# Kernel tuning notes

Hardware: AMD Instinct MI355X
Metric: run time of the kernel (lower is better)

Reference implementation:

```python
import jax, jax.numpy as jnp
import numpy as np

G, N, EPG = 32, 128, 2048   # graphs, nodes/graph (uniform), edges/graph
H, L = 128, 2               # hidden_dim, num_layers
OUT = 12


def setup_inputs() -> dict:
    key = jax.random.key(0)
    ks = jax.random.split(key, 32)
    x = jax.random.randint(ks[0], (G * N, 9), 0, 2, dtype=jnp.int32)
    edge_attr = jax.random.randint(ks[1], (G * EPG, 3), 0, 2, dtype=jnp.int32)
    # edges stay within their own graph (global ids = local + graph offset)
    src = jax.random.randint(ks[2], (G, EPG), 0, N, dtype=jnp.int32)
    dst = jax.random.randint(ks[3], (G, EPG), 0, N, dtype=jnp.int32)
    off = (jnp.arange(G, dtype=jnp.int32) * N)[:, None]
    edge_index = jnp.stack([(src + off).reshape(-1), (dst + off).reshape(-1)]).astype(jnp.int64)
    batch_idx = (jnp.arange(G * N) // N).astype(jnp.int32)

    def p(k, shape, scale=0.05):
        return jax.random.normal(k, shape, dtype=jnp.float32) * scale

    return dict(
        x=x, edge_index=edge_index, edge_attr=edge_attr, batch_idx=batch_idx,
        atom_tab=p(ks[4], (9, 119, H)), bond_tab=p(ks[5], (3, 8, H)),
        W_m1=p(ks[6], (L, 2 * H, H)), b_m1=jnp.zeros((L, H), jnp.float32),
        W_m2=p(ks[7], (L, 2 * H, H)), b_m2=jnp.zeros((L, H), jnp.float32),
        W_me=p(ks[8], (L, H, H)), b_me=jnp.zeros((L, H), jnp.float32),
        W_mg=p(ks[9], (L, H, H)), b_mg=jnp.zeros((L, H), jnp.float32),
        W_h1=p(ks[10], (L, H, H)), b_h1=jnp.zeros((L, H), jnp.float32),
        W_h2=p(ks[11], (L, H, H)), b_h2=jnp.zeros((L, H), jnp.float32),
        W_o1=p(ks[12], (L, 2 * H, H)), b_o1=jnp.zeros((L, H), jnp.float32),
        W_o2=p(ks[13], (L, H, H)), b_o2=jnp.zeros((L, H), jnp.float32),
        Wg1=p(ks[14], (H, H)), bg1=jnp.zeros((H,), jnp.float32),
        Wg2=p(ks[15], (H, OUT)), bg2=jnp.zeros((OUT,), jnp.float32),
    )


def reference(x, edge_index, edge_attr, batch_idx, atom_tab, bond_tab,
              W_m1, b_m1, W_m2, b_m2, W_me, b_me, W_mg, b_mg,
              W_h1, b_h1, W_h2, b_h2, W_o1, b_o1, W_o2, b_o2,
              Wg1, bg1, Wg2, bg2):
    # Atom/Bond encoders: sum of per-feature embeddings
    node_fts = jnp.sum(jax.vmap(lambda t, i: t[i], in_axes=(0, 1))(atom_tab, x), axis=0)        # (G*N, H)
    edge_fts = jnp.sum(jax.vmap(lambda t, i: t[i], in_axes=(0, 1))(bond_tab, edge_attr), axis=0)  # (E, H)

    # dense adjacency + dense edge features (one fused scatter, replaces per-graph loop)
    g = (edge_index[0] // N).astype(jnp.int32)
    s = (edge_index[0] % N).astype(jnp.int32)
    d = (edge_index[1] % N).astype(jnp.int32)
    adj = jnp.zeros((G, N, N), jnp.float32).at[g, s, d].set(1.0)
    edense = jnp.zeros((G, N, N, H), jnp.float32).at[g, s, d].set(edge_fts)

    nd = node_fts.reshape(G, N, H)          # to_dense_batch (uniform graphs -> no padding)
    gf = jnp.zeros((G, H), jnp.float32)
    hid = jnp.zeros_like(nd)
    NEG = jnp.float32(-1e9)

    for l in range(L):  # CLRS MPNN layers
        z = jnp.concatenate([nd, hid], axis=-1)                 # (G, N, 2H)
        m1 = z @ W_m1[l] + b_m1[l]
        m2 = z @ W_m2[l] + b_m2[l]
        me = edense @ W_me[l] + b_me[l]                         # (G, N, N, H)
        mg = gf @ W_mg[l] + b_mg[l]
        msgs = m1[:, None, :, :] + m2[:, :, None, :] + me + mg[:, None, None, :]
        h = jax.nn.relu(msgs)
        h = jax.nn.relu(h @ W_h1[l] + b_h1[l]) @ W_h2[l] + b_h2[l]
        h = jnp.where(adj[..., None] > 0, h, NEG)               # masked max over senders
        agg = jnp.max(h, axis=1)                                # (G, N, H)
        hid = jax.nn.relu(z @ W_o1[l] + b_o1[l] + agg @ W_o2[l] + b_o2[l])

    emb = hid.mean(axis=1)                                      # (G, H)
    return jax.nn.relu(emb @ Wg1 + bg1) @ Wg2 + bg2             # (G, OUT)
```

## Files before the change

### kernel.cpp

```cpp
#include <hip/hip_runtime.h>

#define Gg   32
#define Nn   128
#define Hh   128
#define Ee   65536
#define GN   4096
#define GNN  524288

typedef unsigned short ushort_t;
typedef __attribute__((ext_vector_type(8))) __bf16 bf16x8;
typedef __attribute__((ext_vector_type(4))) float f32x4;
struct us4 { ushort_t a, b, c, d; };

__device__ __forceinline__ float reluf(float x) { return x > 0.f ? x : 0.f; }

__device__ __forceinline__ unsigned fkey(float f) {
  unsigned u = __float_as_uint(f);
  return (u & 0x80000000u) ? ~u : (u | 0x80000000u);
}
__device__ __forceinline__ float funkey(unsigned k) {
  unsigned u = (k & 0x80000000u) ? (k ^ 0x80000000u) : ~k;
  return __uint_as_float(u);
}

__device__ __forceinline__ ushort_t bfh(float x) {
  unsigned u = __float_as_uint(x);
  return (ushort_t)((u + 0x7FFFu + ((u >> 16) & 1u)) >> 16);
}
__device__ __forceinline__ void split2(float x, ushort_t& h, ushort_t& l) {
  h = bfh(x);
  float hf = __uint_as_float(((unsigned)h) << 16);
  l = bfh(x - hf);
}

__global__ __launch_bounds__(128) void k_detect(const int* __restrict__ e32,
                                                int* __restrict__ flag) {
  __shared__ int s;
  if (threadIdx.x == 0) s = 0;
  __syncthreads();
  if (e32[2 * threadIdx.x + 1] != 0) atomicOr(&s, 1);
  __syncthreads();
  if (threadIdx.x == 0) *flag = s;
}

__global__ __launch_bounds__(256) void k_bond_fts(const float* __restrict__ bond_tab,
                                                  float* __restrict__ bf) {
  int t = blockIdx.x * 256 + threadIdx.x;
  int c = t >> 7, h = t & 127;
  int a0 = c & 7, a1 = (c >> 3) & 7, a2 = (c >> 6) & 7;
  bf[t] = bond_tab[(0 * 8 + a0) * Hh + h] + bond_tab[(1 * 8 + a1) * Hh + h] +
          bond_tab[(2 * 8 + a2) * Hh + h];
}

__global__ __launch_bounds__(256) void k_scatter_win(const int* __restrict__ e32,
                                                     const int* __restrict__ flag,
                                                     int* __restrict__ win) {
  int e = blockIdx.x * 256 + threadIdx.x;
  int sg, dg;
  if (*flag) { sg = e32[e]; dg = e32[Ee + e]; }
  else       { sg = e32[2 * e]; dg = e32[2 * Ee + 2 * e]; }
  int g = sg / Nn;
  int s = sg % Nn;
  int d = dg % Nn;
  atomicMax(&win[(g * Nn + d) * Nn + s], e);
}

__global__ __launch_bounds__(256) void k_dcount(const int* __restrict__ win,
                                                int* __restrict__ dcnt) {
  int tid = threadIdx.x;
  int grp = tid >> 7, t = tid & 127;
  int dest = blockIdx.x * 2 + grp;
  bool valid = win[dest * 128 + t] >= 0;
  unsigned long long mask = __ballot(valid);
  __shared__ int cw[4];
  if ((tid & 63) == 0) cw[tid >> 6] = __popcll(mask);
  __syncthreads();
  if (t == 0) dcnt[dest] = cw[grp * 2] + cw[grp * 2 + 1];
}

__global__ __launch_bounds__(512) void k_dscan(const int* __restrict__ dcnt,
                                               int* __restrict__ rowptr) {
  int tid = threadIdx.x;
  int c0, c1, c2, c3, c4, c5, c6, c7;
  int bi = tid * 8;
  c0 = dcnt[bi + 0]; c1 = dcnt[bi + 1]; c2 = dcnt[bi + 2]; c3 = dcnt[bi + 3];
  c4 = dcnt[bi + 4]; c5 = dcnt[bi + 5]; c6 = dcnt[bi + 6]; c7 = dcnt[bi + 7];
  int s = c0 + c1 + c2 + c3 + c4 + c5 + c6 + c7;
  int x = s;
#pragma unroll
  for (int off = 1; off < 64; off <<= 1) {
    int y = __shfl_up(x, off, 64);
    if ((tid & 63) >= off) x += y;
  }
  __shared__ int wsum[8], woff[8];
  if ((tid & 63) == 63) wsum[tid >> 6] = x;
  __syncthreads();
  if (tid == 0) {
    int a = 0;
#pragma unroll
    for (int i = 0; i < 8; ++i) { woff[i] = a; a += wsum[i]; }
  }
  __syncthreads();
  int base = x - s + woff[tid >> 6];
  rowptr[bi + 0] = base; base += c0;
  rowptr[bi + 1] = base; base += c1;
  rowptr[bi + 2] = base; base += c2;
  rowptr[bi + 3] = base; base += c3;
  rowptr[bi + 4] = base; base += c4;
  rowptr[bi + 5] = base; base += c5;
  rowptr[bi + 6] = base; base += c6;
  rowptr[bi + 7] = base; base += c7;
  if (tid == 511) rowptr[4096] = base;
}

__global__ __launch_bounds__(256) void k_dfill(const int* __restrict__ win,
                                               const int* __restrict__ eattr,
                                               const int* __restrict__ rowptr,
                                               unsigned* __restrict__ recs) {
  int tid = threadIdx.x;
  int grp = tid >> 7, t = tid & 127;
  int dest = blockIdx.x * 2 + grp;
  int e = win[dest * 128 + t];
  bool valid = e >= 0;
  unsigned long long mask = __ballot(valid);
  __shared__ int cw[4];
  int lane = tid & 63;
  if (lane == 0) cw[tid >> 6] = __popcll(mask);
  __syncthreads();
  if (valid) {
    int off = __popcll(mask & ((1ull << lane) - 1));
    if ((tid >> 6) & 1) off += cw[grp * 2];
    int a0 = eattr[e * 3 + 0], a1 = eattr[e * 3 + 1], a2 = eattr[e * 3 + 2];
    unsigned code = (unsigned)(a0 + (a1 << 3) + (a2 << 6));
    unsigned idx = ((unsigned)dest << 7) | (unsigned)t;
    recs[rowptr[dest] + off] = (idx << 9) | code;
  }
}


__global__ __launch_bounds__(256) void k_wprep(const float* __restrict__ W_h1,
                                               const float* __restrict__ W_h2,
                                               ushort_t* __restrict__ wt) {
  int t = blockIdx.x * 256 + threadIdx.x;
  int l = t >> 15;
  int m = (t >> 14) & 1;
  int e = t & 16383;
  int n = e & 127, k = e >> 7;
  const float* W = (m == 0 ? W_h1 : W_h2) + l * 16384;
  float v = W[k * 128 + n];
  ushort_t h, lo;
  split2(v, h, lo);
  int nf = n >> 4, lr = n & 15, kf = k >> 5, lg = (k >> 3) & 3, j = k & 7;
  int off = ((nf * 4 + kf) * 64 + lg * 16 + lr) * 8 + j;
  int base = ((l * 2 + m) * 2) * 16384;
  wt[base + off] = h;
  wt[base + 16384 + off] = lo;
}

__global__ __launch_bounds__(256) void k_wprep_o(const float* __restrict__ W_o1,
                                                 const float* __restrict__ W_o2,
                                                 ushort_t* __restrict__ wo) {
  int e = blockIdx.x * 256 + threadIdx.x;
  int l = blockIdx.y;
  int n = e / 384, k = e - n * 384;
  float v = (k < 256) ? W_o1[(l * 256 + k) * 128 + n]
                      : W_o2[(l * 128 + (k - 256)) * 128 + n];
  ushort_t h, lo;
  split2(v, h, lo);
  int nf = n >> 4, lr = n & 15, kf = k >> 5, lg = (k >> 3) & 3, j = k & 7;
  int off = ((nf * 12 + kf) * 64 + lg * 16 + lr) * 8 + j;
  wo[(l * 2 + 0) * 49152 + off] = h;
  wo[(l * 2 + 1) * 49152 + off] = lo;
}

__global__ __launch_bounds__(256) void k_wprep_m(const float* __restrict__ W_m1,
                                                 const float* __restrict__ W_m2,
                                                 ushort_t* __restrict__ wm) {
  int t = blockIdx.x * 256 + threadIdx.x;
  int l = t >> 16;
  int m = (t >> 15) & 1;
  int e = t & 32767;
  int n = e >> 8, k = e & 255;
  const float* W = (m == 0 ? W_m1 : W_m2);
  float v = W[(l * 256 + k) * 128 + n];
  ushort_t h, lo;
  split2(v, h, lo);
  int nf = n >> 4, lr = n & 15, kf = k >> 5, lg = (k >> 3) & 3, j = k & 7;
  int off = ((nf * 8 + kf) * 64 + lg * 16 + lr) * 8 + j;
  int base = ((l * 2 + m) * 2) * 32768;
  wm[base + off] = h;
  wm[base + 32768 + off] = lo;
}

__global__ __launch_bounds__(256) void k_me2(const float* __restrict__ bf,
                                             const float* __restrict__ W_me,
                                             const float* __restrict__ b_me,
                                             const float* __restrict__ b_mg,
                                             float* __restrict__ me0,
                                             float* __restrict__ me1,
                                             unsigned* __restrict__ aggkA,
                                             unsigned* __restrict__ aggkB) {
  int bx = blockIdx.x;
  int l = bx >> 8, b2 = bx & 255;
  const float* W = W_me + l * 16384;
  const float* bme = b_me + l * 128;
  const float* bmg = b_mg + l * 128;
  float* me = l ? me1 : me0;
  unsigned* aggk = l ? aggkB : aggkA;
  __shared__ float v[2][128];
  int tid = threadIdx.x;
  int half = tid >> 7, j = tid & 127;
  int c = b2 * 2 + half;
  v[half][j] = bf[c * 128 + j];
  __syncthreads();
  float acc = bme[j] + bmg[j];
  for (int i = 0; i < 128; ++i) acc += v[half][i] * W[i * 128 + j];
  me[c * 128 + j] = acc;
  unsigned key = fkey(-1.0e9f);
#pragma unroll
  for (int i = 0; i < 8; ++i) aggk[b2 * 2048 + i * 256 + tid] = key;
}

__device__ __forceinline__ void load_afrag(const ushort_t (*MH)[136],
                                           const ushort_t (*ML)[136],
                                           int row, int lg,
                                           bf16x8 ah[4], bf16x8 al[4]) {
#pragma unroll
  for (int kf = 0; kf < 4; ++kf) {
    ah[kf] = *(const bf16x8*)&MH[row][lg * 8 + 32 * kf];
    al[kf] = *(const bf16x8*)&ML[row][lg * 8 + 32 * kf];
  }
}

__device__ __forceinline__ void load_afrag264(const ushort_t (*MH)[264],
                                              const ushort_t (*ML)[264],
                                              int row, int base, int lg,
                                              bf16x8 ah[4], bf16x8 al[4]) {
#pragma unroll
  for (int kf = 0; kf < 4; ++kf) {
    ah[kf] = *(const bf16x8*)&MH[row][base + lg * 8 + 32 * kf];
    al[kf] = *(const bf16x8*)&ML[row][base + lg * 8 + 32 * kf];
  }
}

__global__ __launch_bounds__(256) void k_encode_m12(const int* __restrict__ x,
                                                    const float* __restrict__ atom_tab,
                                                    const ushort_t* __restrict__ wm,
                                                    const float* __restrict__ bi1,
                                                    const float* __restrict__ bi2,
                                                    float* __restrict__ nf_,
                                                    float* __restrict__ hid,
                                                    float* __restrict__ m1,
                                                    float* __restrict__ m2) {
  __shared__ ushort_t AH[16][136];
  __shared__ ushort_t AL[16][136];
  __shared__ int xs[144];
  int tid = threadIdx.x;
  int v0 = blockIdx.x * 16;
  if (tid < 144) xs[tid] = x[v0 * 9 + tid];
  __syncthreads();
#pragma unroll
  for (int i = 0; i < 8; ++i) {
    int e = tid + i * 256;
    int row = e >> 7, col = e & 127;
    float s = 0.f;
#pragma unroll
    for (int f = 0; f < 9; ++f) {
      int idx = xs[row * 9 + f];
      s += atom_tab[(f * 119 + idx) * Hh + col];
    }
    nf_[(v0 + row) * Hh + col] = s;
    hid[(v0 + row) * Hh + col] = 0.f;
    ushort_t h, l;
    split2(s, h, l);
    AH[row][col] = h;
    AL[row][col] = l;
  }
  __syncthreads();
  int lane = tid & 63, wid = tid >> 6;
  int lr = lane & 15, lg = lane >> 4;
  f32x4 a1[2], a2[2];
#pragma unroll
  for (int i = 0; i < 2; ++i) { a1[i] = (f32x4){0.f,0.f,0.f,0.f}; a2[i] = (f32x4){0.f,0.f,0.f,0.f}; }
  const ushort_t* w1h = wm;
  const ushort_t* w1l = wm + 32768;
  const ushort_t* w2h = wm + 65536;
  const ushort_t* w2l = wm + 98304;
  bf16x8 ah[4], al[4];
  load_afrag(AH, AL, lr, lg, ah, al);
#pragma unroll
  for (int jj = 0; jj < 2; ++jj) {
    int nfr = 2 * wid + jj;
#pragma unroll
    for (int kf = 0; kf < 4; ++kf) {
      int ch = ((nfr * 8 + kf) << 9) + lane * 8;
      bf16x8 b1h = *(const bf16x8*)(w1h + ch);
      bf16x8 b1l = *(const bf16x8*)(w1l + ch);
      bf16x8 b2h = *(const bf16x8*)(w2h + ch);
      bf16x8 b2l = *(const bf16x8*)(w2l + ch);
      a1[jj] = __builtin_amdgcn_mfma_f32_16x16x32_bf16(ah[kf], b1h, a1[jj], 0, 0, 0);
      a1[jj] = __builtin_amdgcn_mfma_f32_16x16x32_bf16(ah[kf], b1l, a1[jj], 0, 0, 0);
      a1[jj] = __builtin_amdgcn_mfma_f32_16x16x32_bf16(al[kf], b1h, a1[jj], 0, 0, 0);
      a2[jj] = __builtin_amdgcn_mfma_f32_16x16x32_bf16(ah[kf], b2h, a2[jj], 0, 0, 0);
      a2[jj] = __builtin_amdgcn_mfma_f32_16x16x32_bf16(ah[kf], b2l, a2[jj], 0, 0, 0);
      a2[jj] = __builtin_amdgcn_mfma_f32_16x16x32_bf16(al[kf], b2h, a2[jj], 0, 0, 0);
    }
  }
#pragma unroll
  for (int jj = 0; jj < 2; ++jj) {
    int col = 16 * (2 * wid + jj) + lr;
    float bb1 = bi1[col], bb2 = bi2[col];
#pragma unroll
    for (int reg = 0; reg < 4; ++reg) {
      int row = v0 + lg * 4 + reg;
      m1[row * Hh + col] = a1[jj][reg] + bb1;
      m2[row * Hh + col] = a2[jj][reg] + bb2;
    }
  }
}

__global__ __launch_bounds__(512) void k_edge(const unsigned* __restrict__ recs,
                                              const int* __restrict__ cnt,
                                              const float* __restrict__ m1,
                                              const float* __restrict__ m2,
                                              const float* __restrict__ me,
                                              const ushort_t* __restrict__ wt1h,
                                              const ushort_t* __restrict__ wt1l,
                                              const ushort_t* __restrict__ wt2h,
                                              const ushort_t* __restrict__ wt2l,
                                              const float* __restrict__ b_h1,
                                              const float* __restrict__ b_h2,
                                              unsigned* __restrict__ aggk) {
  __shared__ ushort_t MH[64][136];
  __shared__ ushort_t ML[64][136];
  __shared__ unsigned srec[64];
  int tid = threadIdx.x;
  int n = *cnt;
  if (tid < 64) {
    int r = blockIdx.x * 64 + tid;
    srec[tid] = (r < n) ? recs[r] : 0xFFFFFFFFu;
  }
  __syncthreads();
  {
    int c4 = tid & 31, rq = tid >> 5;
#pragma unroll
    for (int i = 0; i < 4; ++i) {
      int r = 16 * i + rq;
      float4 v = make_float4(0.f, 0.f, 0.f, 0.f);
      unsigned rec = srec[r];
      if (rec != 0xFFFFFFFFu) {
        int code = rec & 511;
        unsigned idx = rec >> 9;
        int s = idx & 127, d = (idx >> 7) & 127, g = idx >> 14;
        float4 a = *(const float4*)(m1 + (((g << 7) + d) << 7) + c4 * 4);
        float4 b = *(const float4*)(m2 + (((g << 7) + s) << 7) + c4 * 4);
        float4 cme = *(const float4*)(me + (code << 7) + c4 * 4);
        v.x = reluf(a.x + b.x + cme.x);
        v.y = reluf(a.y + b.y + cme.y);
        v.z = reluf(a.z + b.z + cme.z);
        v.w = reluf(a.w + b.w + cme.w);
      }
      us4 h4, l4;
      split2(v.x, h4.a, l4.a); split2(v.y, h4.b, l4.b);
      split2(v.z, h4.c, l4.c); split2(v.w, h4.d, l4.d);
      *(us4*)&MH[r][c4 * 4] = h4;
      *(us4*)&ML[r][c4 * 4] = l4;
    }
  }
  __syncthreads();

  int lane = tid & 63, wid = tid >> 6;
  int lr = lane & 15, lg = lane >> 4;
  float b1v = b_h1[16 * wid + lr];
  float b2v = b_h2[16 * wid + lr];
  f32x4 acc[4];
#pragma unroll
  for (int rg = 0; rg < 4; ++rg) acc[rg] = (f32x4){0.f, 0.f, 0.f, 0.f};
#pragma unroll
  for (int rg = 0; rg < 4; ++rg) {
    bf16x8 ah[4], al[4];
    load_afrag(MH, ML, 16 * rg + lr, lg, ah, al);
#pragma unroll
    for (int kf = 0; kf < 4; ++kf) {
      int ch = ((wid * 4 + kf) << 9) + lane * 8;
      bf16x8 bh = *(const bf16x8*)(wt1h + ch);
      bf16x8 bl = *(const bf16x8*)(wt1l + ch);
      acc[rg] = __builtin_amdgcn_mfma_f32_16x16x32_bf16(ah[kf], bh, acc[rg], 0, 0, 0);
      acc[rg] = __builtin_amdgcn_mfma_f32_16x16x32_bf16(ah[kf], bl, acc[rg], 0, 0, 0);
      acc[rg] = __builtin_amdgcn_mfma_f32_16x16x32_bf16(al[kf], bh, acc[rg], 0, 0, 0);
    }
  }
  __syncthreads();
#pragma unroll
  for (int rg = 0; rg < 4; ++rg)
#pragma unroll
    for (int reg = 0; reg < 4; ++reg) {
      float t = reluf(acc[rg][reg] + b1v);
      int row = 16 * rg + lg * 4 + reg;
      int col = 16 * wid + lr;
      ushort_t h, l;
      split2(t, h, l);
      MH[row][col] = h;
      ML[row][col] = l;
    }
  __syncthreads();
#pragma unroll
  for (int rg = 0; rg < 4; ++rg) acc[rg] = (f32x4){0.f, 0.f, 0.f, 0.f};
#pragma unroll
  for (int rg = 0; rg < 4; ++rg) {
    bf16x8 ah[4], al[4];
    load_afrag(MH, ML, 16 * rg + lr, lg, ah, al);
#pragma unroll
    for (int kf = 0; kf < 4; ++kf) {
      int ch = ((wid * 4 + kf) << 9) + lane * 8;
      bf16x8 bh = *(const bf16x8*)(wt2h + ch);
      bf16x8 bl = *(const bf16x8*)(wt2l + ch);
      acc[rg] = __builtin_amdgcn_mfma_f32_16x16x32_bf16(ah[kf], bh, acc[rg], 0, 0, 0);
      acc[rg] = __builtin_amdgcn_mfma_f32_16x16x32_bf16(ah[kf], bl, acc[rg], 0, 0, 0);
      acc[rg] = __builtin_amdgcn_mfma_f32_16x16x32_bf16(al[kf], bh, acc[rg], 0, 0, 0);
    }
  }
  __syncthreads();
#pragma unroll
  for (int rg = 0; rg < 4; ++rg)
#pragma unroll
    for (int reg = 0; reg < 4; ++reg) {
      int row = 16 * rg + lg * 4 + reg;
      int col = 16 * wid + lr;
      unsigned b = __float_as_uint(acc[rg][reg] + b2v);
      MH[row][col] = (ushort_t)(b >> 16);
      ML[row][col] = (ushort_t)(b & 0xFFFFu);
    }
  __syncthreads();
  {
    int c = tid & 127, quarter = tid >> 7;
    int rbeg = quarter * 16, rend = rbeg + 16;
    unsigned curkey = 0xFFFFu;
    float best = -3.0e38f;
    for (int r = rbeg; r < rend; ++r) {
      unsigned rec = srec[r];
      unsigned key = rec >> 16;
      if (key != curkey) {
        if (curkey != 0xFFFFu)
          atomicMax(aggk + (curkey << 7) + c, fkey(best));
        curkey = key;
        best = -3.0e38f;
      }
      if (key != 0xFFFFu) {
        unsigned b = ((unsigned)MH[r][c] << 16) | (unsigned)ML[r][c];
        best = fmaxf(best, __uint_as_float(b));
      }
    }
    if (curkey != 0xFFFFu)
      atomicMax(aggk + (curkey << 7) + c, fkey(best));
  }
}

__global__ __launch_bounds__(256) void k_out(const float* __restrict__ nf,
                                             const float* __restrict__ hid,
                                             const unsigned* __restrict__ aggk,
                                             const ushort_t* __restrict__ wo_h,
                                             const ushort_t* __restrict__ wo_l,
                                             const float* __restrict__ bo1,
                                             const float* __restrict__ bo2,
                                             float* __restrict__ hidn) {
  __shared__ ushort_t MH[16][136];
  __shared__ ushort_t ML[16][136];
  int tid = threadIdx.x;
  int v0 = blockIdx.x * 16;
  int lane = tid & 63, wid = tid >> 6;
  int lr = lane & 15, lg = lane >> 4;
  f32x4 acc[2];
#pragma unroll
  for (int jj = 0; jj < 2; ++jj) acc[jj] = (f32x4){0.f, 0.f, 0.f, 0.f};

  for (int seg = 0; seg < 3; ++seg) {
#pragma unroll
    for (int i = 0; i < 2; ++i) {
      int idx = tid + i * 256;
      int row = idx >> 5, c4 = idx & 31;
      float4 v;
      if (seg == 0)      v = ((const float4*)nf)[(v0 + row) * 32 + c4];
      else if (seg == 1) v = ((const float4*)hid)[(v0 + row) * 32 + c4];
      else {
        uint4 k4 = ((const uint4*)aggk)[(v0 + row) * 32 + c4];
        v.x = funkey(k4.x); v.y = funkey(k4.y); v.z = funkey(k4.z); v.w = funkey(k4.w);
      }
      us4 h4, l4;
      split2(v.x, h4.a, l4.a);
      split2(v.y, h4.b, l4.b);
      split2(v.z, h4.c, l4.c);
      split2(v.w, h4.d, l4.d);
      *(us4*)&MH[row][c4 * 4] = h4;
      *(us4*)&ML[row][c4 * 4] = l4;
    }
    __syncthreads();
    bf16x8 ah[4], al[4];
    load_afrag(MH, ML, lr, lg, ah, al);
#pragma unroll
    for (int jj = 0; jj < 2; ++jj) {
      int nfr = 2 * wid + jj;
#pragma unroll
      for (int kf = 0; kf < 4; ++kf) {
        int ch = ((nfr * 12 + seg * 4 + kf) << 9) + lane * 8;
        bf16x8 bh = *(const bf16x8*)(wo_h + ch);
        bf16x8 bl = *(const bf16x8*)(wo_l + ch);
        acc[jj] = __builtin_amdgcn_mfma_f32_16x16x32_bf16(ah[kf], bh, acc[jj], 0, 0, 0);
        acc[jj] = __builtin_amdgcn_mfma_f32_16x16x32_bf16(ah[kf], bl, acc[jj], 0, 0, 0);
        acc[jj] = __builtin_amdgcn_mfma_f32_16x16x32_bf16(al[kf], bh, acc[jj], 0, 0, 0);
      }
    }
    __syncthreads();
  }
#pragma unroll
  for (int jj = 0; jj < 2; ++jj) {
    int col = 16 * (2 * wid + jj) + lr;
    float b = bo1[col] + bo2[col];
#pragma unroll
    for (int reg = 0; reg < 4; ++reg)
      hidn[(v0 + lg * 4 + reg) * Hh + col] = reluf(acc[jj][reg] + b);
  }
}

__global__ __launch_bounds__(256) void k_out_m12(const float* __restrict__ nf,
                                                 const float* __restrict__ hid,
                                                 const unsigned* __restrict__ aggk,
                                                 const ushort_t* __restrict__ wo_h,
                                                 const ushort_t* __restrict__ wo_l,
                                                 const float* __restrict__ bo1,
                                                 const float* __restrict__ bo2,
                                                 const ushort_t* __restrict__ wm,
                                                 const float* __restrict__ bm1,
                                                 const float* __restrict__ bm2,
                                                 float* __restrict__ hidn,
                                                 float* __restrict__ m1,
                                                 float* __restrict__ m2) {
  __shared__ ushort_t AH[16][264];
  __shared__ ushort_t AL[16][264];
  int tid = threadIdx.x;
  int v0 = blockIdx.x * 16;
  int lane = tid & 63, wid = tid >> 6;
  int lr = lane & 15, lg = lane >> 4;
  f32x4 acc[2];
#pragma unroll
  for (int jj = 0; jj < 2; ++jj) acc[jj] = (f32x4){0.f, 0.f, 0.f, 0.f};

  for (int seg = 0; seg < 3; ++seg) {
#pragma unroll
    for (int i = 0; i < 2; ++i) {
      int idx = tid + i * 256;
      int row = idx >> 5, c4 = idx & 31;
      float4 v;
      if (seg == 0)      v = ((const float4*)nf)[(v0 + row) * 32 + c4];
      else if (seg == 1) v = ((const float4*)hid)[(v0 + row) * 32 + c4];
      else {
        uint4 k4 = ((const uint4*)aggk)[(v0 + row) * 32 + c4];
        v.x = funkey(k4.x); v.y = funkey(k4.y); v.z = funkey(k4.z); v.w = funkey(k4.w);
      }
      us4 h4, l4;
      split2(v.x, h4.a, l4.a);
      split2(v.y, h4.b, l4.b);
      split2(v.z, h4.c, l4.c);
      split2(v.w, h4.d, l4.d);
      *(us4*)&AH[row][c4 * 4] = h4;
      *(us4*)&AL[row][c4 * 4] = l4;
    }
    __syncthreads();
    bf16x8 ah[4], al[4];
    load_afrag264(AH, AL, lr, 0, lg, ah, al);
#pragma unroll
    for (int jj = 0; jj < 2; ++jj) {
      int nfr = 2 * wid + jj;
#pragma unroll
      for (int kf = 0; kf < 4; ++kf) {
        int ch = ((nfr * 12 + seg * 4 + kf) << 9) + lane * 8;
        bf16x8 bh = *(const bf16x8*)(wo_h + ch);
        bf16x8 bl = *(const bf16x8*)(wo_l + ch);
        acc[jj] = __builtin_amdgcn_mfma_f32_16x16x32_bf16(ah[kf], bh, acc[jj], 0, 0, 0);
        acc[jj] = __builtin_amdgcn_mfma_f32_16x16x32_bf16(ah[kf], bl, acc[jj], 0, 0, 0);
        acc[jj] = __builtin_amdgcn_mfma_f32_16x16x32_bf16(al[kf], bh, acc[jj], 0, 0, 0);
      }
    }
    __syncthreads();
  }
#pragma unroll
  for (int jj = 0; jj < 2; ++jj) {
    int col = 16 * (2 * wid + jj) + lr;
    float b = bo1[col] + bo2[col];
#pragma unroll
    for (int reg = 0; reg < 4; ++reg) {
      float hv = reluf(acc[jj][reg] + b);
      int row = lg * 4 + reg;
      hidn[(v0 + row) * Hh + col] = hv;
      ushort_t h, l;
      split2(hv, h, l);
      AH[row][128 + col] = h;
      AL[row][128 + col] = l;
    }
  }
#pragma unroll
  for (int i = 0; i < 2; ++i) {
    int idx = tid + i * 256;
    int row = idx >> 5, c4 = idx & 31;
    float4 v = ((const float4*)nf)[(v0 + row) * 32 + c4];
    us4 h4, l4;
    split2(v.x, h4.a, l4.a);
    split2(v.y, h4.b, l4.b);
    split2(v.z, h4.c, l4.c);
    split2(v.w, h4.d, l4.d);
    *(us4*)&AH[row][c4 * 4] = h4;
    *(us4*)&AL[row][c4 * 4] = l4;
  }
  __syncthreads();
  f32x4 a1[2], a2[2];
#pragma unroll
  for (int i = 0; i < 2; ++i) { a1[i] = (f32x4){0.f,0.f,0.f,0.f}; a2[i] = (f32x4){0.f,0.f,0.f,0.f}; }
  const ushort_t* w1h = wm;
  const ushort_t* w1l = wm + 32768;
  const ushort_t* w2h = wm + 65536;
  const ushort_t* w2l = wm + 98304;
#pragma unroll
  for (int seg = 0; seg < 2; ++seg) {
    bf16x8 ah[4], al[4];
    load_afrag264(AH, AL, lr, seg * 128, lg, ah, al);
#pragma unroll
    for (int jj = 0; jj < 2; ++jj) {
      int nfr = 2 * wid + jj;
#pragma unroll
      for (int kf = 0; kf < 4; ++kf) {
        int ch = ((nfr * 8 + seg * 4 + kf) << 9) + lane * 8;
        bf16x8 b1h = *(const bf16x8*)(w1h + ch);
        bf16x8 b1l = *(const bf16x8*)(w1l + ch);
        bf16x8 b2h = *(const bf16x8*)(w2h + ch);
        bf16x8 b2l = *(const bf16x8*)(w2l + ch);
        a1[jj] = __builtin_amdgcn_mfma_f32_16x16x32_bf16(ah[kf], b1h, a1[jj], 0, 0, 0);
        a1[jj] = __builtin_amdgcn_mfma_f32_16x16x32_bf16(ah[kf], b1l, a1[jj], 0, 0, 0);
        a1[jj] = __builtin_amdgcn_mfma_f32_16x16x32_bf16(al[kf], b1h, a1[jj], 0, 0, 0);
        a2[jj] = __builtin_amdgcn_mfma_f32_16x16x32_bf16(ah[kf], b2h, a2[jj], 0, 0, 0);
        a2[jj] = __builtin_amdgcn_mfma_f32_16x16x32_bf16(ah[kf], b2l, a2[jj], 0, 0, 0);
        a2[jj] = __builtin_amdgcn_mfma_f32_16x16x32_bf16(al[kf], b2h, a2[jj], 0, 0, 0);
      }
    }
  }
#pragma unroll
  for (int jj = 0; jj < 2; ++jj) {
    int col = 16 * (2 * wid + jj) + lr;
    float bb1 = bm1[col], bb2 = bm2[col];
#pragma unroll
    for (int reg = 0; reg < 4; ++reg) {
      int row = v0 + lg * 4 + reg;
      m1[row * Hh + col] = a1[jj][reg] + bb1;
      m2[row * Hh + col] = a2[jj][reg] + bb2;
    }
  }
}

__global__ __launch_bounds__(128) void k_head(const float* __restrict__ hid,
                                              const float* __restrict__ Wg1,
                                              const float* __restrict__ bg1,
                                              const float* __restrict__ Wg2,
                                              const float* __restrict__ bg2,
                                              float* __restrict__ out) {
  __shared__ float emb[Hh];
  __shared__ float tt[Hh];
  int g = blockIdx.x, j = threadIdx.x;
  float s = 0.f;
  for (int n = 0; n < Nn; ++n) s += hid[(g * Nn + n) * Hh + j];
  emb[j] = s * (1.f / Nn);
  __syncthreads();
  float a = bg1[j];
  for (int i = 0; i < Hh; ++i) a += emb[i] * Wg1[i * Hh + j];
  tt[j] = reluf(a);
  __syncthreads();
  if (j < 12) {
    float o = bg2[j];
    for (int i = 0; i < Hh; ++i) o += tt[i] * Wg2[i * 12 + j];
    out[g * 12 + j] = o;
  }
}

extern "C" void kernel_launch(void* const* d_in, const int* in_sizes, int n_in,
                              void* d_out, int out_size, void* d_ws, size_t ws_size,
                              hipStream_t stream) {
  const int* x = (const int*)d_in[0];
  const int* eidx32 = (const int*)d_in[1];
  const int* eattr = (const int*)d_in[2];
  const float* atom_tab = (const float*)d_in[4];
  const float* bond_tab = (const float*)d_in[5];
  const float* W_m1 = (const float*)d_in[6];
  const float* b_m1 = (const float*)d_in[7];
  const float* W_m2 = (const float*)d_in[8];
  const float* b_m2 = (const float*)d_in[9];
  const float* W_me = (const float*)d_in[10];
  const float* b_me = (const float*)d_in[11];
  const float* b_mg = (const float*)d_in[13];
  const float* W_h1 = (const float*)d_in[14];
  const float* b_h1 = (const float*)d_in[15];
  const float* W_h2 = (const float*)d_in[16];
  const float* b_h2 = (const float*)d_in[17];
  const float* W_o1 = (const float*)d_in[18];
  const float* b_o1 = (const float*)d_in[19];
  const float* W_o2 = (const float*)d_in[20];
  const float* b_o2 = (const float*)d_in[21];
  const float* Wg1 = (const float*)d_in[22];
  const float* bg1 = (const float*)d_in[23];
  const float* Wg2 = (const float*)d_in[24];
  const float* bg2 = (const float*)d_in[25];
  float* out = (float*)d_out;

  char* ws = (char*)d_ws;
  float* nf = (float*)(ws);
  float* hidA = (float*)(ws + (2u << 20));
  float* hidB = (float*)(ws + (4u << 20));
  float* m1 = (float*)(ws + (6u << 20));
  float* m2 = (float*)(ws + (8u << 20));
  unsigned* aggkA = (unsigned*)(ws + (10u << 20));
  int* win = (int*)(ws + (12u << 20));
  ushort_t* wt = (ushort_t*)(ws + (14u << 20));
  float* bf = (float*)(ws + (14u << 20) + (256u << 10));
  float* me0 = (float*)(ws + (14u << 20) + (512u << 10));
  float* me1 = (float*)(ws + (14u << 20) + (768u << 10));
  unsigned* recs = (unsigned*)(ws + (15u << 20));
  int* dcnt = (int*)(ws + (15u << 20) + (256u << 10));
  int* rowptr = (int*)(ws + (15u << 20) + (272u << 10));
  int* eflag = (int*)(ws + (15u << 20) + (304u << 10));
  unsigned* aggkB = (unsigned*)(ws + (16u << 20));
  ushort_t* wo = (ushort_t*)(ws + (18u << 20));
  ushort_t* wm = (ushort_t*)(ws + (18u << 20) + (512u << 10));

  hipMemsetAsync(win, 0xFF, GNN * sizeof(int), stream);
  k_detect<<<1, 128, 0, stream>>>(eidx32, eflag);
  k_bond_fts<<<256, 256, 0, stream>>>(bond_tab, bf);
  k_wprep<<<256, 256, 0, stream>>>(W_h1, W_h2, wt);
  k_wprep_o<<<dim3(192, 2), 256, 0, stream>>>(W_o1, W_o2, wo);
  k_wprep_m<<<512, 256, 0, stream>>>(W_m1, W_m2, wm);
  k_me2<<<512, 256, 0, stream>>>(bf, W_me, b_me, b_mg, me0, me1, aggkA, aggkB);
  k_encode_m12<<<256, 256, 0, stream>>>(x, atom_tab, wm, b_m1, b_m2,
                                        nf, hidA, m1, m2);
  k_scatter_win<<<256, 256, 0, stream>>>(eidx32, eflag, win);
  k_dcount<<<2048, 256, 0, stream>>>(win, dcnt);
  k_dscan<<<1, 512, 0, stream>>>(dcnt, rowptr);
  k_dfill<<<2048, 256, 0, stream>>>(win, eattr, rowptr, recs);

  int* cnt = rowptr + 4096;

  k_edge<<<1024, 512, 0, stream>>>(recs, cnt, m1, m2, me0,
                                   wt + 0 * 16384, wt + 1 * 16384,
                                   wt + 2 * 16384, wt + 3 * 16384,
                                   b_h1, b_h2, aggkA);
  k_out_m12<<<256, 256, 0, stream>>>(nf, hidA, aggkA,
                                     wo + 0 * 49152, wo + 1 * 49152,
                                     b_o1, b_o2,
                                     wm + 131072, b_m1 + Hh, b_m2 + Hh,
                                     hidB, m1, m2);
  k_edge<<<1024, 512, 0, stream>>>(recs, cnt, m1, m2, me1,
                                   wt + 4 * 16384, wt + 5 * 16384,
                                   wt + 6 * 16384, wt + 7 * 16384,
                                   b_h1 + Hh, b_h2 + Hh, aggkB);
  k_out<<<256, 256, 0, stream>>>(nf, hidB, aggkB,
                                 wo + 2 * 49152, wo + 3 * 49152,
                                 b_o1 + Hh, b_o2 + Hh, hidA);
  k_head<<<32, 128, 0, stream>>>(hidA, Wg1, bg1, Wg2, bg2, out);
}
```

Measured before the change: 127.6 us.

## Fuse preprocessing kernels and replace count/scan/fill with atomic-append compaction

Merges the three weight-prep kernels and the adjacency-window memset into one launch, and folds the edge-format detection into the scatter kernel and the bond-feature sum into k_me2. It replaces the dcount/dscan/dfill pipeline with a single fill kernel that reserves output slots through an atomicAdd on a global counter. Together these remove several launches and their serialization gaps. In exchange, the record order becomes nondeterministic across runs, and k_edge must tolerate records that are no longer grouped in destination order.

```diff
diff --git a/kernel.cpp b/kernel.cpp
--- a/kernel.cpp
+++ b/kernel.cpp
@@ -33,31 +33,80 @@
   l = bfh(x - hf);
 }
 
-__global__ __launch_bounds__(128) void k_detect(const int* __restrict__ e32,
-                                                int* __restrict__ flag) {
-  __shared__ int s;
-  if (threadIdx.x == 0) s = 0;
-  __syncthreads();
-  if (e32[2 * threadIdx.x + 1] != 0) atomicOr(&s, 1);
-  __syncthreads();
-  if (threadIdx.x == 0) *flag = s;
-}
-
-__global__ __launch_bounds__(256) void k_bond_fts(const float* __restrict__ bond_tab,
-                                                  float* __restrict__ bf) {
-  int t = blockIdx.x * 256 + threadIdx.x;
-  int c = t >> 7, h = t & 127;
-  int a0 = c & 7, a1 = (c >> 3) & 7, a2 = (c >> 6) & 7;
-  bf[t] = bond_tab[(0 * 8 + a0) * Hh + h] + bond_tab[(1 * 8 + a1) * Hh + h] +
-          bond_tab[(2 * 8 + a2) * Hh + h];
+__global__ __launch_bounds__(256) void k_wprep_all(const float* __restrict__ W_h1,
+                                                   const float* __restrict__ W_h2,
+                                                   const float* __restrict__ W_o1,
+                                                   const float* __restrict__ W_o2,
+                                                   const float* __restrict__ W_m1,
+                                                   const float* __restrict__ W_m2,
+                                                   ushort_t* __restrict__ wt,
+                                                   ushort_t* __restrict__ wo,
+                                                   ushort_t* __restrict__ wm,
+                                                   int* __restrict__ win,
+                                                   int* __restrict__ cnt) {
+  int b = blockIdx.x;
+  int tid = threadIdx.x;
+  if (b < 256) {
+    int t = b * 256 + tid;
+    int l = t >> 15;
+    int m = (t >> 14) & 1;
+    int e = t & 16383;
+    int n = e & 127, k = e >> 7;
+    const float* W = (m == 0 ? W_h1 : W_h2) + l * 16384;
+    float v = W[k * 128 + n];
+    ushort_t h, lo;
+    split2(v, h, lo);
+    int nf = n >> 4, lr = n & 15, kf = k >> 5, lg = (k >> 3) & 3, j = k & 7;
+    int off = ((nf * 4 + kf) * 64 + lg * 16 + lr) * 8 + j;
+    int base = ((l * 2 + m) * 2) * 16384;
+    wt[base + off] = h;
+    wt[base + 16384 + off] = lo;
+  } else if (b < 640) {
+    int ep = (b - 256) * 256 + tid;
+    int l = (ep >= 49152) ? 1 : 0;
+    int e = ep - l * 49152;
+    int n = e / 384, k = e - n * 384;
+    float v = (k < 256) ? W_o1[(l * 256 + k) * 128 + n]
+                        : W_o2[(l * 128 + (k - 256)) * 128 + n];
+    ushort_t h, lo;
+    split2(v, h, lo);
+    int nf = n >> 4, lr = n & 15, kf = k >> 5, lg = (k >> 3) & 3, j = k & 7;
+    int off = ((nf * 12 + kf) * 64 + lg * 16 + lr) * 8 + j;
+    wo[(l * 2 + 0) * 49152 + off] = h;
+    wo[(l * 2 + 1) * 49152 + off] = lo;
+  } else if (b < 1152) {
+    int t = (b - 640) * 256 + tid;
+    int l = t >> 16;
+    int m = (t >> 15) & 1;
+    int e = t & 32767;
+    int n = e >> 8, k = e & 255;
+    const float* W = (m == 0 ? W_m1 : W_m2);
+    float v = W[(l * 256 + k) * 128 + n];
+    ushort_t h, lo;
+    split2(v, h, lo);
+    int nf = n >> 4, lr = n & 15, kf = k >> 5, lg = (k >> 3) & 3, j = k & 7;
+    int off = ((nf * 8 + kf) * 64 + lg * 16 + lr) * 8 + j;
+    int base = ((l * 2 + m) * 2) * 32768;
+    wm[base + off] = h;
+    wm[base + 32768 + off] = lo;
+  } else {
+    int idx = (b - 1152) * 256 + tid;
+    ((int4*)win)[idx] = make_int4(-1, -1, -1, -1);
+    if (idx == 0) *cnt = 0;
+  }
 }
 
 __global__ __launch_bounds__(256) void k_scatter_win(const int* __restrict__ e32,
-                                                     const int* __restrict__ flag,
                                                      int* __restrict__ win) {
-  int e = blockIdx.x * 256 + threadIdx.x;
+  __shared__ int sflag;
+  int tid = threadIdx.x;
+  if (tid == 0) sflag = 0;
+  __syncthreads();
+  if (tid < 128 && e32[2 * tid + 1] != 0) atomicOr(&sflag, 1);
+  __syncthreads();
+  int e = blockIdx.x * 256 + tid;
   int sg, dg;
-  if (*flag) { sg = e32[e]; dg = e32[Ee + e]; }
+  if (sflag) { sg = e32[e]; dg = e32[Ee + e]; }
   else       { sg = e32[2 * e]; dg = e32[2 * Ee + 2 * e]; }
   int g = sg / Nn;
   int s = sg % Nn;
@@ -65,58 +114,10 @@
   atomicMax(&win[(g * Nn + d) * Nn + s], e);
 }
 
-__global__ __launch_bounds__(256) void k_dcount(const int* __restrict__ win,
-                                                int* __restrict__ dcnt) {
-  int tid = threadIdx.x;
-  int grp = tid >> 7, t = tid & 127;
-  int dest = blockIdx.x * 2 + grp;
-  bool valid = win[dest * 128 + t] >= 0;
-  unsigned long long mask = __ballot(valid);
-  __shared__ int cw[4];
-  if ((tid & 63) == 0) cw[tid >> 6] = __popcll(mask);
-  __syncthreads();
-  if (t == 0) dcnt[dest] = cw[grp * 2] + cw[grp * 2 + 1];
-}
-
-__global__ __launch_bounds__(512) void k_dscan(const int* __restrict__ dcnt,
-                                               int* __restrict__ rowptr) {
-  int tid = threadIdx.x;
-  int c0, c1, c2, c3, c4, c5, c6, c7;
-  int bi = tid * 8;
-  c0 = dcnt[bi + 0]; c1 = dcnt[bi + 1]; c2 = dcnt[bi + 2]; c3 = dcnt[bi + 3];
-  c4 = dcnt[bi + 4]; c5 = dcnt[bi + 5]; c6 = dcnt[bi + 6]; c7 = dcnt[bi + 7];
-  int s = c0 + c1 + c2 + c3 + c4 + c5 + c6 + c7;
-  int x = s;
-#pragma unroll
-  for (int off = 1; off < 64; off <<= 1) {
-    int y = __shfl_up(x, off, 64);
-    if ((tid & 63) >= off) x += y;
-  }
-  __shared__ int wsum[8], woff[8];
-  if ((tid & 63) == 63) wsum[tid >> 6] = x;
-  __syncthreads();
-  if (tid == 0) {
-    int a = 0;
-#pragma unroll
-    for (int i = 0; i < 8; ++i) { woff[i] = a; a += wsum[i]; }
-  }
-  __syncthreads();
-  int base = x - s + woff[tid >> 6];
-  rowptr[bi + 0] = base; base += c0;
-  rowptr[bi + 1] = base; base += c1;
-  rowptr[bi + 2] = base; base += c2;
-  rowptr[bi + 3] = base; base += c3;
-  rowptr[bi + 4] = base; base += c4;
-  rowptr[bi + 5] = base; base += c5;
-  rowptr[bi + 6] = base; base += c6;
-  rowptr[bi + 7] = base; base += c7;
-  if (tid == 511) rowptr[4096] = base;
-}
-
-__global__ __launch_bounds__(256) void k_dfill(const int* __restrict__ win,
-                                               const int* __restrict__ eattr,
-                                               const int* __restrict__ rowptr,
-                                               unsigned* __restrict__ recs) {
+__global__ __launch_bounds__(256) void k_dfill2(const int* __restrict__ win,
+                                                const int* __restrict__ eattr,
+                                                int* __restrict__ cnt,
+                                                unsigned* __restrict__ recs) {
   int tid = threadIdx.x;
   int grp = tid >> 7, t = tid & 127;
   int dest = blockIdx.x * 2 + grp;
@@ -124,75 +125,27 @@
   bool valid = e >= 0;
   unsigned long long mask = __ballot(valid);
   __shared__ int cw[4];
-  int lane = tid & 63;
-  if (lane == 0) cw[tid >> 6] = __popcll(mask);
+  __shared__ int sbase;
+  int lane = tid & 63, wv = tid >> 6;
+  if (lane == 0) cw[wv] = __popcll(mask);
+  __syncthreads();
+  if (tid == 0) {
+    int tot = cw[0] + cw[1] + cw[2] + cw[3];
+    sbase = tot ? atomicAdd(cnt, tot) : 0;
+  }
   __syncthreads();
   if (valid) {
     int off = __popcll(mask & ((1ull << lane) - 1));
-    if ((tid >> 6) & 1) off += cw[grp * 2];
+    if (wv & 1) off += cw[grp * 2];
+    if (grp) off += cw[0] + cw[1];
     int a0 = eattr[e * 3 + 0], a1 = eattr[e * 3 + 1], a2 = eattr[e * 3 + 2];
     unsigned code = (unsigned)(a0 + (a1 << 3) + (a2 << 6));
     unsigned idx = ((unsigned)dest << 7) | (unsigned)t;
-    recs[rowptr[dest] + off] = (idx << 9) | code;
-  }
-}
-
-
-__global__ __launch_bounds__(256) void k_wprep(const float* __restrict__ W_h1,
-                                               const float* __restrict__ W_h2,
-                                               ushort_t* __restrict__ wt) {
-  int t = blockIdx.x * 256 + threadIdx.x;
-  int l = t >> 15;
-  int m = (t >> 14) & 1;
-  int e = t & 16383;
-  int n = e & 127, k = e >> 7;
-  const float* W = (m == 0 ? W_h1 : W_h2) + l * 16384;
-  float v = W[k * 128 + n];
-  ushort_t h, lo;
-  split2(v, h, lo);
-  int nf = n >> 4, lr = n & 15, kf = k >> 5, lg = (k >> 3) & 3, j = k & 7;
-  int off = ((nf * 4 + kf) * 64 + lg * 16 + lr) * 8 + j;
-  int base = ((l * 2 + m) * 2) * 16384;
-  wt[base + off] = h;
-  wt[base + 16384 + off] = lo;
-}
-
-__global__ __launch_bounds__(256) void k_wprep_o(const float* __restrict__ W_o1,
-                                                 const float* __restrict__ W_o2,
-                                                 ushort_t* __restrict__ wo) {
-  int e = blockIdx.x * 256 + threadIdx.x;
-  int l = blockIdx.y;
-  int n = e / 384, k = e - n * 384;
-  float v = (k < 256) ? W_o1[(l * 256 + k) * 128 + n]
-                      : W_o2[(l * 128 + (k - 256)) * 128 + n];
-  ushort_t h, lo;
-  split2(v, h, lo);
-  int nf = n >> 4, lr = n & 15, kf = k >> 5, lg = (k >> 3) & 3, j = k & 7;
-  int off = ((nf * 12 + kf) * 64 + lg * 16 + lr) * 8 + j;
-  wo[(l * 2 + 0) * 49152 + off] = h;
-  wo[(l * 2 + 1) * 49152 + off] = lo;
-}
-
-__global__ __launch_bounds__(256) void k_wprep_m(const float* __restrict__ W_m1,
-                                                 const float* __restrict__ W_m2,
-                                                 ushort_t* __restrict__ wm) {
-  int t = blockIdx.x * 256 + threadIdx.x;
-  int l = t >> 16;
-  int m = (t >> 15) & 1;
-  int e = t & 32767;
-  int n = e >> 8, k = e & 255;
-  const float* W = (m == 0 ? W_m1 : W_m2);
-  float v = W[(l * 256 + k) * 128 + n];
-  ushort_t h, lo;
-  split2(v, h, lo);
-  int nf = n >> 4, lr = n & 15, kf = k >> 5, lg = (k >> 3) & 3, j = k & 7;
-  int off = ((nf * 8 + kf) * 64 + lg * 16 + lr) * 8 + j;
-  int base = ((l * 2 + m) * 2) * 32768;
-  wm[base + off] = h;
-  wm[base + 32768 + off] = lo;
-}
-
-__global__ __launch_bounds__(256) void k_me2(const float* __restrict__ bf,
+    recs[sbase + off] = (idx << 9) | code;
+  }
+}
+
+__global__ __launch_bounds__(256) void k_me2(const float* __restrict__ bond_tab,
                                              const float* __restrict__ W_me,
                                              const float* __restrict__ b_me,
                                              const float* __restrict__ b_mg,
@@ -211,7 +164,9 @@
   int tid = threadIdx.x;
   int half = tid >> 7, j = tid & 127;
   int c = b2 * 2 + half;
-  v[half][j] = bf[c * 128 + j];
+  int a0 = c & 7, a1 = (c >> 3) & 7, a2 = (c >> 6) & 7;
+  v[half][j] = bond_tab[a0 * 128 + j] + bond_tab[(8 + a1) * 128 + j] +
+               bond_tab[(16 + a2) * 128 + j];
   __syncthreads();
   float acc = bme[j] + bmg[j];
   for (int i = 0; i < 128; ++i) acc += v[half][i] * W[i * 128 + j];
@@ -717,32 +672,21 @@
   unsigned* aggkA = (unsigned*)(ws + (10u << 20));
   int* win = (int*)(ws + (12u << 20));
   ushort_t* wt = (ushort_t*)(ws + (14u << 20));
-  float* bf = (float*)(ws + (14u << 20) + (256u << 10));
-  float* me0 = (float*)(ws + (14u << 20) + (512u << 10));
-  float* me1 = (float*)(ws + (14u << 20) + (768u << 10));
+  float* me0 = (float*)(ws + (14u << 20) + (256u << 10));
+  float* me1 = (float*)(ws + (14u << 20) + (512u << 10));
   unsigned* recs = (unsigned*)(ws + (15u << 20));
-  int* dcnt = (int*)(ws + (15u << 20) + (256u << 10));
-  int* rowptr = (int*)(ws + (15u << 20) + (272u << 10));
-  int* eflag = (int*)(ws + (15u << 20) + (304u << 10));
+  int* cnt = (int*)(ws + (15u << 20) + (256u << 10));
   unsigned* aggkB = (unsigned*)(ws + (16u << 20));
   ushort_t* wo = (ushort_t*)(ws + (18u << 20));
   ushort_t* wm = (ushort_t*)(ws + (18u << 20) + (512u << 10));
 
-  hipMemsetAsync(win, 0xFF, GNN * sizeof(int), stream);
-  k_detect<<<1, 128, 0, stream>>>(eidx32, eflag);
-  k_bond_fts<<<256, 256, 0, stream>>>(bond_tab, bf);
-  k_wprep<<<256, 256, 0, stream>>>(W_h1, W_h2, wt);
-  k_wprep_o<<<dim3(192, 2), 256, 0, stream>>>(W_o1, W_o2, wo);
-  k_wprep_m<<<512, 256, 0, stream>>>(W_m1, W_m2, wm);
-  k_me2<<<512, 256, 0, stream>>>(bf, W_me, b_me, b_mg, me0, me1, aggkA, aggkB);
+  k_wprep_all<<<1664, 256, 0, stream>>>(W_h1, W_h2, W_o1, W_o2, W_m1, W_m2,
+                                        wt, wo, wm, win, cnt);
+  k_me2<<<512, 256, 0, stream>>>(bond_tab, W_me, b_me, b_mg, me0, me1, aggkA, aggkB);
   k_encode_m12<<<256, 256, 0, stream>>>(x, atom_tab, wm, b_m1, b_m2,
                                         nf, hidA, m1, m2);
-  k_scatter_win<<<256, 256, 0, stream>>>(eidx32, eflag, win);
-  k_dcount<<<2048, 256, 0, stream>>>(win, dcnt);
-  k_dscan<<<1, 512, 0, stream>>>(dcnt, rowptr);
-  k_dfill<<<2048, 256, 0, stream>>>(win, eattr, rowptr, recs);
-
-  int* cnt = rowptr + 4096;
+  k_scatter_win<<<256, 256, 0, stream>>>(eidx32, win);
+  k_dfill2<<<2048, 256, 0, stream>>>(win, eattr, cnt, recs);
 
   k_edge<<<1024, 512, 0, stream>>>(recs, cnt, m1, m2, me0,
                                    wt + 0 * 16384, wt + 1 * 16384,
```

Result: slower. 134.5 us (+5.4%).
